# Kernel tuning notes

Hardware: AMD Instinct MI355X
Metric: run time of the kernel (lower is better)

## Reference

```python
import jax, jax.numpy as jnp
import numpy as np

N_NODES = 50000
N_EDGES = 100000
TOKENS = 10000
D = 32
EDGE_TYPES = 8
STEPS = 5


def setup_inputs() -> dict:
    key = jax.random.key(0)
    ks = jax.random.split(key, 12)
    token = jax.random.randint(ks[0], (N_NODES,), 0, TOKENS)
    etype = jax.random.randint(ks[1], (N_EDGES,), 0, EDGE_TYPES)
    src = jax.random.randint(ks[2], (N_EDGES,), 0, N_NODES)
    dst = jax.random.randint(ks[3], (N_EDGES,), 0, N_NODES)
    s = 1.0 / np.sqrt(D)
    emb = jax.random.normal(ks[4], (TOKENS, D), jnp.float32)
    # per-edge-type weights: [T, D, D, 2] (fwd/reverse message transforms)
    W_edge = jax.random.normal(ks[5], (EDGE_TYPES, D, D, 2), jnp.float32) * s
    W_r = jax.random.normal(ks[6], (3 * D, D), jnp.float32) * s
    b_r = jnp.zeros((D,), jnp.float32)
    W_z = jax.random.normal(ks[7], (3 * D, D), jnp.float32) * s
    b_z = jnp.zeros((D,), jnp.float32)
    W_t = jax.random.normal(ks[8], (3 * D, D), jnp.float32) * s
    b_t = jnp.zeros((D,), jnp.float32)
    return {"token": token, "etype": etype, "src": src, "dst": dst,
            "emb": emb, "W_edge": W_edge, "W_r": W_r, "b_r": b_r,
            "W_z": W_z, "b_z": b_z, "W_t": W_t, "b_t": b_t}


def reference(token, etype, src, dst, emb, W_edge, W_r, b_r, W_z, b_z, W_t, b_t):
    n = token.shape[0]
    prop = emb[token]                       # [N, D]
    We = W_edge[etype]                      # [E, D, D, 2] gathered per edge (once)
    for _ in range(STEPS):
        h_src = prop[src]                   # [E, D] gather source states
        # src_mul_edge + sum over src dim == per-edge matmul: [E,D,2]
        fea = jnp.einsum('ei,eijk->ejk', h_src, We)
        in_fea = jax.ops.segment_sum(fea[:, :, 0], dst, num_segments=n)   # [N, D]
        out_fea = jax.ops.segment_sum(fea[:, :, 1], src, num_segments=n)  # [N, D]
        cat = jnp.concatenate([in_fea, out_fea, prop], axis=1)            # [N, 3D]
        r = jax.nn.sigmoid(cat @ W_r + b_r)
        z = jax.nn.sigmoid(cat @ W_z + b_z)
        cat2 = jnp.concatenate([in_fea, out_fea, r * prop], axis=1)
        h_hat = jnp.tanh(cat2 @ W_t + b_t)
        prop = (1.0 - z) * prop + z * h_hat
    return prop
```

## Files before the change

### kernel.cpp

```cpp
#include <hip/hip_runtime.h>

#define N_NODES 50000
#define N_EDGES 100000
#define DD 32
#define STEPS 5
#define ETYPES 8
#define CAP_T 13312
#define CAP (ETYPES * CAP_T)
#define TRASH N_EDGES
#define SCAN_B 49

#define GRU_GRID ((N_NODES / 16 + 3) / 4)

typedef float f32x4v __attribute__((ext_vector_type(4)));
typedef short s16x8 __attribute__((ext_vector_type(8)));
typedef ushort u16x8 __attribute__((ext_vector_type(8)));
typedef unsigned long long u64;

__device__ __forceinline__ ushort f2bf(float x) {
    unsigned u = __float_as_uint(x);
    u += 0x7fff + ((u >> 16) & 1);
    return (ushort)(u >> 16);
}
__device__ __forceinline__ float bf2f(ushort h) {
    return __uint_as_float(((unsigned)h) << 16);
}
__device__ __forceinline__ void mk_split(const float* v, s16x8& h, s16x8& lo) {
#pragma unroll
    for (int i = 0; i < 8; ++i) {
        ushort hi = f2bf(v[i]);
        h[i] = (short)hi;
        lo[i] = (short)f2bf(v[i] - bf2f(hi));
    }
}
__device__ __forceinline__ float sigm(float x) {
    return 1.f / (1.f + __expf(-x));
}
__device__ __forceinline__ float fast_tanh(float x) {
    x = fminf(fmaxf(x, -15.f), 15.f);
    float e = __expf(2.f * x);
    return (e - 1.f) / (e + 1.f);
}

__global__ void init_kernel(const int* __restrict__ token,
                            const float* __restrict__ emb,
                            float* __restrict__ prop,
                            int* __restrict__ cnt,
                            u64* __restrict__ c8,
                            int* __restrict__ se,
                            int* __restrict__ spi) {
    int idx = blockIdx.x * 256 + threadIdx.x;
    int n = idx >> 5, j = idx & 31;
    prop[idx] = emb[token[n] * DD + j];
    if (idx < N_NODES + ETYPES) cnt[idx] = 0;
    if (idx < N_NODES) c8[idx] = 0ull;
    if (idx < CAP) { se[idx] = 0; spi[idx] = TRASH; }
}

__global__ __launch_bounds__(256) void
wfrag_kernel(const float* __restrict__ W_edge,
             const float* __restrict__ W_r, const float* __restrict__ W_z,
             const float* __restrict__ W_t,
             ushort* __restrict__ wfh, ushort* __restrict__ wfl,
             ushort* __restrict__ wgh, ushort* __restrict__ wgl) {
    int idx = blockIdx.x * 256 + threadIdx.x;
    if (idx < ETYPES * 4 * 64) {
        int t  = idx >> 8;
        int nt = (idx >> 6) & 3;
        int l  = idx & 63;
        int n  = nt * 16 + (l & 15);
        int j  = n & 31;
        int p  = n >> 5;
#pragma unroll
        for (int i = 0; i < 8; ++i) {
            int k = (l >> 4) * 8 + i;
            float v = W_edge[(((size_t)t * DD + k) * DD + j) * 2 + p];
            ushort hi = f2bf(v);
            int o = ((t * 4 + nt) * 64 + l) * 8 + i;
            wfh[o] = hi;
            wfl[o] = f2bf(v - bf2f(hi));
        }
    } else if (idx < ETYPES * 4 * 64 + 1152) {
        int x = idx - ETYPES * 4 * 64;
        int g  = x / 384;
        int kt = (x / 128) % 3;
        int nt = (x / 64) % 2;
        int l  = x & 63;
        const float* W = g == 0 ? W_r : (g == 1 ? W_z : W_t);
        int col = nt * 16 + (l & 15);
#pragma unroll
        for (int i = 0; i < 8; ++i) {
            int k = kt * 32 + (l >> 4) * 8 + i;
            float v = W[k * DD + col];
            ushort hi = f2bf(v);
            int o = (((g * 3 + kt) * 2 + nt) * 64 + l) * 8 + i;
            wgh[o] = hi;
            wgl[o] = f2bf(v - bf2f(hi));
        }
    }
}

__global__ void hist_kernel(const int* __restrict__ etype,
                            const int* __restrict__ src,
                            const int* __restrict__ dst,
                            int* __restrict__ cnt_in, int* __restrict__ tcnt,
                            u64* __restrict__ c8,
                            int* __restrict__ rank_in, int* __restrict__ qe) {
    __shared__ int lh[ETYPES], lbase[ETYPES];
    int tid = threadIdx.x;
    int e = blockIdx.x * 256 + tid;
    if (tid < ETYPES) lh[tid] = 0;
    __syncthreads();
    int t = 0, lr = 0;
    bool v = e < N_EDGES;
    if (v) {
        t = etype[e];
        lr = atomicAdd(&lh[t], 1);
        rank_in[e] = atomicAdd(&cnt_in[dst[e]], 1);
        atomicAdd(&c8[src[e]], 1ull << (8 * t));
    }
    __syncthreads();
    if (tid < ETYPES) lbase[tid] = atomicAdd(&tcnt[tid], lh[tid]);
    __syncthreads();
    if (v) qe[e] = t * CAP_T + lbase[t] + lr;
}

__global__ __launch_bounds__(1024) void
scan1(const int* __restrict__ cnt_in, int* __restrict__ off_in,
      int* __restrict__ bsum) {
    __shared__ int s[1024];
    int i = blockIdx.x * 1024 + threadIdx.x;
    int x = (i < N_NODES) ? cnt_in[i] : 0;
    s[threadIdx.x] = x;
    __syncthreads();
    for (int ofs = 1; ofs < 1024; ofs <<= 1) {
        int u = (threadIdx.x >= ofs) ? s[threadIdx.x - ofs] : 0;
        __syncthreads();
        s[threadIdx.x] += u;
        __syncthreads();
    }
    if (i < N_NODES) off_in[i] = s[threadIdx.x] - x;
    if (threadIdx.x == 1023) bsum[blockIdx.x] = s[1023];
}

__global__ void scan2(const int* __restrict__ bsum, int* __restrict__ ebase,
                      int* __restrict__ off_in) {
    __shared__ int s[64];
    int t = threadIdx.x;
    int x = (t < SCAN_B) ? bsum[t] : 0;
    s[t] = x;
    __syncthreads();
    for (int ofs = 1; ofs < 64; ofs <<= 1) {
        int u = (t >= ofs) ? s[t - ofs] : 0;
        __syncthreads();
        s[t] += u;
        __syncthreads();
    }
    if (t < SCAN_B) ebase[t] = s[t] - x;
    if (t == 0) off_in[N_NODES] = N_EDGES;
}

__global__ __launch_bounds__(1024) void
scan3(int* __restrict__ off_in, const int* __restrict__ ebase) {
    int i = blockIdx.x * 1024 + threadIdx.x;
    if (i < N_NODES) off_in[i] += ebase[blockIdx.x];
}

__global__ void place_kernel(const int* __restrict__ src,
                             const int* __restrict__ dst,
                             const int* __restrict__ in_off,
                             const int* __restrict__ rank_in,
                             const int* __restrict__ qe,
                             int* __restrict__ se, int* __restrict__ spi) {
    int e = blockIdx.x * 256 + threadIdx.x;
    if (e < N_EDGES) {
        int q = qe[e];
        if (q < CAP) {
            se[q]  = src[e];
            spi[q] = in_off[dst[e]] + rank_in[e];
        }
    }
}

__global__ __launch_bounds__(256) void
edge_kernel(const int* __restrict__ se, const int* __restrict__ spi,
            const ushort* __restrict__ wfh, const ushort* __restrict__ wfl,
            const float* __restrict__ prop,
            ushort* __restrict__ fea_in) {
    int wv = blockIdx.x * 4 + (threadIdx.x >> 6);
    int l  = threadIdx.x & 63;
    int slot0 = wv * 16;
    int type = slot0 / CAP_T;
    int m  = l & 15;
    int kb = l >> 4;

    int sm = se[slot0 + m];
    const float4* p4 = (const float4*)prop;
    float4 h0 = p4[(size_t)sm * 8 + kb * 2];
    float4 h1 = p4[(size_t)sm * 8 + kb * 2 + 1];
    float hv[8] = {h0.x, h0.y, h0.z, h0.w, h1.x, h1.y, h1.z, h1.w};
    s16x8 ah, al;
    mk_split(hv, ah, al);

    int pr[4];
#pragma unroll
    for (int reg = 0; reg < 4; ++reg) pr[reg] = spi[slot0 + kb * 4 + reg];

    const s16x8* bh8 = (const s16x8*)wfh;
    const s16x8* bl8 = (const s16x8*)wfl;
    f32x4v acc[2];
#pragma unroll
    for (int nt = 0; nt < 2; ++nt) {
        s16x8 bh = bh8[(type * 4 + nt) * 64 + l];
        s16x8 bl = bl8[(type * 4 + nt) * 64 + l];
        f32x4v a = {0.f, 0.f, 0.f, 0.f};
        a = __builtin_amdgcn_mfma_f32_16x16x32_bf16(ah, bh, a, 0, 0, 0);
        a = __builtin_amdgcn_mfma_f32_16x16x32_bf16(al, bh, a, 0, 0, 0);
        a = __builtin_amdgcn_mfma_f32_16x16x32_bf16(ah, bl, a, 0, 0, 0);
        acc[nt] = a;
    }
#pragma unroll
    for (int nt = 0; nt < 2; ++nt)
#pragma unroll
        for (int reg = 0; reg < 4; ++reg)
            fea_in[(size_t)pr[reg] * DD + nt * 16 + m] = f2bf(acc[nt][reg]);
}

__global__ __launch_bounds__(256) void
gru_kernel(const ushort* __restrict__ wgh, const ushort* __restrict__ wgl,
           const ushort* __restrict__ wfh, const ushort* __restrict__ wfl,
           const float* __restrict__ b_r, const float* __restrict__ b_z,
           const float* __restrict__ b_t,
           const ushort* __restrict__ fea_in,
           const int* __restrict__ in_off,
           const u64* __restrict__ c8,
           float* __restrict__ prop,
           float* __restrict__ out2) {
    __shared__ float tr[4][16 * 36];
    const int wvl = threadIdx.x >> 6;
    const int wv = blockIdx.x * 4 + wvl;
    if (wv * 16 >= N_NODES) return;
    const int l = threadIdx.x & 63;
    const int m = l & 15;
    const int kb = l >> 4;
    const int gn = wv * 16 + m;

    int i0 = in_off[gn], i1 = in_off[gn + 1];
    u64 cb[4];
#pragma unroll
    for (int reg = 0; reg < 4; ++reg) cb[reg] = c8[wv * 16 + kb * 4 + reg];
    float pA[8];
    {
        const float4* p4 = (const float4*)prop;
        float4 a = p4[(size_t)gn * 8 + kb * 2];
        float4 b = p4[(size_t)gn * 8 + kb * 2 + 1];
        pA[0] = a.x; pA[1] = a.y; pA[2] = a.z; pA[3] = a.w;
        pA[4] = b.x; pA[5] = b.y; pA[6] = b.z; pA[7] = b.w;
    }
    s16x8 ph, pl;
    mk_split(pA, ph, pl);

    const s16x8* eh8 = (const s16x8*)wfh;
    const s16x8* el8 = (const s16x8*)wfl;
    f32x4v outD[2];
    outD[0] = (f32x4v){0.f, 0.f, 0.f, 0.f};
    outD[1] = (f32x4v){0.f, 0.f, 0.f, 0.f};
#pragma unroll 1
    for (int t = 0; t < ETYPES; ++t) {
        s16x8 bh2 = eh8[(t * 4 + 2) * 64 + l];
        s16x8 bl2 = el8[(t * 4 + 2) * 64 + l];
        s16x8 bh3 = eh8[(t * 4 + 3) * 64 + l];
        s16x8 bl3 = el8[(t * 4 + 3) * 64 + l];
        f32x4v a0 = {0.f, 0.f, 0.f, 0.f}, a1 = {0.f, 0.f, 0.f, 0.f};
        a0 = __builtin_amdgcn_mfma_f32_16x16x32_bf16(ph, bh2, a0, 0, 0, 0);
        a0 = __builtin_amdgcn_mfma_f32_16x16x32_bf16(pl, bh2, a0, 0, 0, 0);
        a0 = __builtin_amdgcn_mfma_f32_16x16x32_bf16(ph, bl2, a0, 0, 0, 0);
        a1 = __builtin_amdgcn_mfma_f32_16x16x32_bf16(ph, bh3, a1, 0, 0, 0);
        a1 = __builtin_amdgcn_mfma_f32_16x16x32_bf16(pl, bh3, a1, 0, 0, 0);
        a1 = __builtin_amdgcn_mfma_f32_16x16x32_bf16(ph, bl3, a1, 0, 0, 0);
#pragma unroll
        for (int reg = 0; reg < 4; ++reg) {
            float w = (float)((cb[reg] >> (8 * t)) & 0xff);
            outD[0][reg] = fmaf(w, a0[reg], outD[0][reg]);
            outD[1][reg] = fmaf(w, a1[reg], outD[1][reg]);
        }
    }

    float va[8];
#pragma unroll
    for (int i = 0; i < 8; ++i) va[i] = 0.f;
    {
        const u16x8* fi8 = (const u16x8*)fea_in;
        for (int r = i0; r < i1; ++r) {
            u16x8 x = fi8[(size_t)r * 4 + kb];
#pragma unroll
            for (int i = 0; i < 8; ++i) va[i] += bf2f(x[i]);
        }
    }

    float* T = tr[wvl];
#pragma unroll
    for (int nt = 0; nt < 2; ++nt)
#pragma unroll
        for (int reg = 0; reg < 4; ++reg)
            T[(kb * 4 + reg) * 36 + nt * 16 + m] = outD[nt][reg];
    float oA[8];
    {
        const float4* T4 = (const float4*)(T + m * 36 + kb * 8);
        float4 x = T4[0], y = T4[1];
        oA[0] = x.x; oA[1] = x.y; oA[2] = x.z; oA[3] = x.w;
        oA[4] = y.x; oA[5] = y.y; oA[6] = y.z; oA[7] = y.w;
    }

    s16x8 ah[3], al[3];
    mk_split(va, ah[0], al[0]);
    mk_split(oA, ah[1], al[1]);
    ah[2] = ph; al[2] = pl;

    const s16x8* bh8 = (const s16x8*)wgh;
    const s16x8* bl8 = (const s16x8*)wgl;
    f32x4v ar[2], az[2], at_[2];
#pragma unroll
    for (int nt = 0; nt < 2; ++nt) {
        ar[nt] = (f32x4v){0.f, 0.f, 0.f, 0.f};
        az[nt] = (f32x4v){0.f, 0.f, 0.f, 0.f};
        at_[nt] = (f32x4v){0.f, 0.f, 0.f, 0.f};
    }
#pragma unroll
    for (int nt = 0; nt < 2; ++nt) {
#pragma unroll
        for (int kt = 0; kt < 3; ++kt) {
            s16x8 bh = bh8[((0 * 3 + kt) * 2 + nt) * 64 + l];
            s16x8 bl = bl8[((0 * 3 + kt) * 2 + nt) * 64 + l];
            ar[nt] = __builtin_amdgcn_mfma_f32_16x16x32_bf16(ah[kt], bh, ar[nt], 0, 0, 0);
            ar[nt] = __builtin_amdgcn_mfma_f32_16x16x32_bf16(al[kt], bh, ar[nt], 0, 0, 0);
            ar[nt] = __builtin_amdgcn_mfma_f32_16x16x32_bf16(ah[kt], bl, ar[nt], 0, 0, 0);
            s16x8 ch = bh8[((1 * 3 + kt) * 2 + nt) * 64 + l];
            s16x8 cl = bl8[((1 * 3 + kt) * 2 + nt) * 64 + l];
            az[nt] = __builtin_amdgcn_mfma_f32_16x16x32_bf16(ah[kt], ch, az[nt], 0, 0, 0);
            az[nt] = __builtin_amdgcn_mfma_f32_16x16x32_bf16(al[kt], ch, az[nt], 0, 0, 0);
            az[nt] = __builtin_amdgcn_mfma_f32_16x16x32_bf16(ah[kt], cl, az[nt], 0, 0, 0);
            if (kt < 2) {
                s16x8 th = bh8[((2 * 3 + kt) * 2 + nt) * 64 + l];
                s16x8 tl = bl8[((2 * 3 + kt) * 2 + nt) * 64 + l];
                at_[nt] = __builtin_amdgcn_mfma_f32_16x16x32_bf16(ah[kt], th, at_[nt], 0, 0, 0);
                at_[nt] = __builtin_amdgcn_mfma_f32_16x16x32_bf16(al[kt], th, at_[nt], 0, 0, 0);
                at_[nt] = __builtin_amdgcn_mfma_f32_16x16x32_bf16(ah[kt], tl, at_[nt], 0, 0, 0);
            }
        }
    }

    float rv[2][4], zv[2][4], pD[2][4];
#pragma unroll
    for (int nt = 0; nt < 2; ++nt) {
        float br = b_r[nt * 16 + m];
        float bz = b_z[nt * 16 + m];
#pragma unroll
        for (int reg = 0; reg < 4; ++reg) {
            int nd = wv * 16 + kb * 4 + reg;
            pD[nt][reg] = prop[(size_t)nd * DD + nt * 16 + m];
            rv[nt][reg] = sigm(ar[nt][reg] + br) * pD[nt][reg];
            zv[nt][reg] = sigm(az[nt][reg] + bz);
        }
    }

#pragma unroll
    for (int nt = 0; nt < 2; ++nt)
#pragma unroll
        for (int reg = 0; reg < 4; ++reg)
            T[(kb * 4 + reg) * 36 + nt * 16 + m] = rv[nt][reg];
    float rpA[8];
    {
        const float4* T4 = (const float4*)(T + m * 36 + kb * 8);
        float4 x = T4[0], y = T4[1];
        rpA[0] = x.x; rpA[1] = x.y; rpA[2] = x.z; rpA[3] = x.w;
        rpA[4] = y.x; rpA[5] = y.y; rpA[6] = y.z; rpA[7] = y.w;
    }
    s16x8 rh, rl;
    mk_split(rpA, rh, rl);
#pragma unroll
    for (int nt = 0; nt < 2; ++nt) {
        s16x8 th = bh8[((2 * 3 + 2) * 2 + nt) * 64 + l];
        s16x8 tl = bl8[((2 * 3 + 2) * 2 + nt) * 64 + l];
        at_[nt] = __builtin_amdgcn_mfma_f32_16x16x32_bf16(rh, th, at_[nt], 0, 0, 0);
        at_[nt] = __builtin_amdgcn_mfma_f32_16x16x32_bf16(rl, th, at_[nt], 0, 0, 0);
        at_[nt] = __builtin_amdgcn_mfma_f32_16x16x32_bf16(rh, tl, at_[nt], 0, 0, 0);
    }

#pragma unroll
    for (int nt = 0; nt < 2; ++nt) {
        float bt = b_t[nt * 16 + m];
#pragma unroll
        for (int reg = 0; reg < 4; ++reg) {
            int nd = wv * 16 + kb * 4 + reg;
            float tv = fast_tanh(at_[nt][reg] + bt);
            float o = fmaf(zv[nt][reg], tv - pD[nt][reg], pD[nt][reg]);
            if (out2) out2[(size_t)nd * DD + nt * 16 + m] = o;
            else      prop[(size_t)nd * DD + nt * 16 + m] = o;
        }
    }
}

extern "C" void kernel_launch(void* const* d_in, const int* in_sizes, int n_in,
                              void* d_out, int out_size, void* d_ws, size_t ws_size,
                              hipStream_t stream) {
    const int*   token  = (const int*)d_in[0];
    const int*   etype  = (const int*)d_in[1];
    const int*   src    = (const int*)d_in[2];
    const int*   dst    = (const int*)d_in[3];
    const float* emb    = (const float*)d_in[4];
    const float* W_edge = (const float*)d_in[5];
    const float* W_r    = (const float*)d_in[6];
    const float* b_r    = (const float*)d_in[7];
    const float* W_z    = (const float*)d_in[8];
    const float* b_z    = (const float*)d_in[9];
    const float* W_t    = (const float*)d_in[10];
    const float* b_t    = (const float*)d_in[11];
    float* out = (float*)d_out;

    float* prop      = (float*)d_ws;
    ushort* fea_in   = (ushort*)(prop + (size_t)N_NODES * DD);
    ushort* wfh = fea_in + (size_t)(N_EDGES + 1) * DD;
    ushort* wfl = wfh + ETYPES * 4 * 64 * 8;
    ushort* wgh = wfl + ETYPES * 4 * 64 * 8;
    ushort* wgl = wgh + 1152 * 8;
    u64* c8     = (u64*)(wgl + 1152 * 8);
    int* in_off   = (int*)(c8 + N_NODES);
    int* se       = in_off + (N_NODES + 1);
    int* spi      = se + CAP;

    int* cnt      = (int*)fea_in;
    int* cnt_in   = cnt;
    int* tcnt     = cnt + N_NODES;
    int* rank_in  = cnt + N_NODES + ETYPES;
    int* qe       = rank_in + N_EDGES;
    int* bsum     = qe + N_EDGES;
    int* ebase    = bsum + SCAN_B;

    init_kernel<<<(N_NODES * DD) / 256, 256, 0, stream>>>(token, emb, prop, cnt,
                                                          c8, se, spi);
    wfrag_kernel<<<13, 256, 0, stream>>>(W_edge, W_r, W_z, W_t,
                                         wfh, wfl, wgh, wgl);
    hist_kernel<<<(N_EDGES + 255) / 256, 256, 0, stream>>>(
        etype, src, dst, cnt_in, tcnt, c8, rank_in, qe);
    scan1<<<SCAN_B, 1024, 0, stream>>>(cnt_in, in_off, bsum);
    scan2<<<1, 64, 0, stream>>>(bsum, ebase, in_off);
    scan3<<<SCAN_B, 1024, 0, stream>>>(in_off, ebase);
    place_kernel<<<(N_EDGES + 255) / 256, 256, 0, stream>>>(
        src, dst, in_off, rank_in, qe, se, spi);

    for (int step = 0; step < STEPS; ++step) {
        edge_kernel<<<CAP / 64, 256, 0, stream>>>(se, spi, wfh, wfl, prop,
                                                  fea_in);
        gru_kernel<<<GRU_GRID, 256, 0, stream>>>(
            wgh, wgl, wfh, wfl, b_r, b_z, b_t, fea_in, in_off, c8,
            prop, (step == STEPS - 1) ? out : nullptr);
    }
}
```

Before: 232.4 us.

## Bucket edges within each type by source-node block to improve gather locality

Edges were previously placed into per-type slots in arbitrary atomic order. They are now counted into 256 source-node buckets per type, an extra single-block scan kernel turns those counts into offsets, and each edge is placed in source-block order within its type. The aim is locality: consecutive edges in edge_kernel should gather prop rows from nearby source nodes, so the 5 repeated gathers hit cache more often. The cost is one more kernel launch, global atomics on 2048 counters instead of shared-memory ones, and a dependency of the per-type CAP_T capacity on this ordering.

New measurement: 247.9 us. +6.7%, slower.

```diff
diff --git a/kernel.cpp b/kernel.cpp
--- a/kernel.cpp
+++ b/kernel.cpp
@@ -9,6 +9,7 @@
 #define CAP (ETYPES * CAP_T)
 #define TRASH N_EDGES
 #define SCAN_B 49
+#define NSB 256
 
 #define GRU_GRID ((N_NODES / 16 + 3) / 4)
 
@@ -52,7 +53,7 @@
     int idx = blockIdx.x * 256 + threadIdx.x;
     int n = idx >> 5, j = idx & 31;
     prop[idx] = emb[token[n] * DD + j];
-    if (idx < N_NODES + ETYPES) cnt[idx] = 0;
+    if (idx < N_NODES + ETYPES * NSB) cnt[idx] = 0;
     if (idx < N_NODES) c8[idx] = 0ull;
     if (idx < CAP) { se[idx] = 0; spi[idx] = TRASH; }
 }
@@ -103,26 +104,43 @@
 __global__ void hist_kernel(const int* __restrict__ etype,
                             const int* __restrict__ src,
                             const int* __restrict__ dst,
-                            int* __restrict__ cnt_in, int* __restrict__ tcnt,
+                            int* __restrict__ cnt_in, int* __restrict__ tsb,
                             u64* __restrict__ c8,
-                            int* __restrict__ rank_in, int* __restrict__ qe) {
-    __shared__ int lh[ETYPES], lbase[ETYPES];
-    int tid = threadIdx.x;
-    int e = blockIdx.x * 256 + tid;
-    if (tid < ETYPES) lh[tid] = 0;
+                            int* __restrict__ rank_in, int* __restrict__ rb) {
+    int e = blockIdx.x * 256 + threadIdx.x;
+    if (e < N_EDGES) {
+        int t = etype[e];
+        int s = src[e];
+        rank_in[e] = atomicAdd(&cnt_in[dst[e]], 1);
+        rb[e] = atomicAdd(&tsb[t * NSB + (s >> 8)], 1);
+        atomicAdd(&c8[s], 1ull << (8 * t));
+    }
+}
+
+__global__ __launch_bounds__(256) void
+scanT(const int* __restrict__ tsb, int* __restrict__ qoff) {
+    __shared__ int s[256];
+    __shared__ int tstart[ETYPES];
+    int ti = threadIdx.x;
+    int base = ti * 8;
+    int loc[8];
+    int ls = 0;
+#pragma unroll
+    for (int i = 0; i < 8; ++i) { loc[i] = ls; ls += tsb[base + i]; }
+    s[ti] = ls;
     __syncthreads();
-    int t = 0, lr = 0;
-    bool v = e < N_EDGES;
-    if (v) {
-        t = etype[e];
-        lr = atomicAdd(&lh[t], 1);
-        rank_in[e] = atomicAdd(&cnt_in[dst[e]], 1);
-        atomicAdd(&c8[src[e]], 1ull << (8 * t));
-    }
+    for (int ofs = 1; ofs < 256; ofs <<= 1) {
+        int u = (ti >= ofs) ? s[ti - ofs] : 0;
+        __syncthreads();
+        s[ti] += u;
+        __syncthreads();
+    }
+    int ebase = s[ti] - ls;
+    if ((ti & 31) == 0) tstart[ti >> 5] = ebase;
     __syncthreads();
-    if (tid < ETYPES) lbase[tid] = atomicAdd(&tcnt[tid], lh[tid]);
-    __syncthreads();
-    if (v) qe[e] = t * CAP_T + lbase[t] + lr;
+    int tb = tstart[ti >> 5];
+#pragma unroll
+    for (int i = 0; i < 8; ++i) qoff[base + i] = ebase + loc[i] - tb;
 }
 
 __global__ __launch_bounds__(1024) void
@@ -166,17 +184,21 @@
     if (i < N_NODES) off_in[i] += ebase[blockIdx.x];
 }
 
-__global__ void place_kernel(const int* __restrict__ src,
+__global__ void place_kernel(const int* __restrict__ etype,
+                             const int* __restrict__ src,
                              const int* __restrict__ dst,
                              const int* __restrict__ in_off,
                              const int* __restrict__ rank_in,
-                             const int* __restrict__ qe,
+                             const int* __restrict__ rb,
+                             const int* __restrict__ qoff,
                              int* __restrict__ se, int* __restrict__ spi) {
     int e = blockIdx.x * 256 + threadIdx.x;
     if (e < N_EDGES) {
-        int q = qe[e];
+        int t = etype[e];
+        int s = src[e];
+        int q = t * CAP_T + qoff[t * NSB + (s >> 8)] + rb[e];
         if (q < CAP) {
-            se[q]  = src[e];
+            se[q]  = s;
             spi[q] = in_off[dst[e]] + rank_in[e];
         }
     }
@@ -431,10 +453,11 @@
 
     int* cnt      = (int*)fea_in;
     int* cnt_in   = cnt;
-    int* tcnt     = cnt + N_NODES;
-    int* rank_in  = cnt + N_NODES + ETYPES;
-    int* qe       = rank_in + N_EDGES;
-    int* bsum     = qe + N_EDGES;
+    int* tsb      = cnt + N_NODES;
+    int* rank_in  = tsb + ETYPES * NSB;
+    int* rb       = rank_in + N_EDGES;
+    int* qoff     = rb + N_EDGES;
+    int* bsum     = qoff + ETYPES * NSB;
     int* ebase    = bsum + SCAN_B;
 
     init_kernel<<<(N_NODES * DD) / 256, 256, 0, stream>>>(token, emb, prop, cnt,
@@ -442,12 +465,13 @@
     wfrag_kernel<<<13, 256, 0, stream>>>(W_edge, W_r, W_z, W_t,
                                          wfh, wfl, wgh, wgl);
     hist_kernel<<<(N_EDGES + 255) / 256, 256, 0, stream>>>(
-        etype, src, dst, cnt_in, tcnt, c8, rank_in, qe);
+        etype, src, dst, cnt_in, tsb, c8, rank_in, rb);
+    scanT<<<1, 256, 0, stream>>>(tsb, qoff);
     scan1<<<SCAN_B, 1024, 0, stream>>>(cnt_in, in_off, bsum);
     scan2<<<1, 64, 0, stream>>>(bsum, ebase, in_off);
     scan3<<<SCAN_B, 1024, 0, stream>>>(in_off, ebase);
     place_kernel<<<(N_EDGES + 255) / 256, 256, 0, stream>>>(
-        src, dst, in_off, rank_in, qe, se, spi);
+        etype, src, dst, in_off, rank_in, rb, qoff, se, spi);
 
     for (int step = 0; step < STEPS; ++step) {
         edge_kernel<<<CAP / 64, 256, 0, stream>>>(se, spi, wfh, wfl, prop,
```
